# Optimization experiments

Hardware: AMD Instinct MI355X
Metric: run time of the kernel (lower is better)

The kernel has to match this reference:

```python
import jax, jax.numpy as jnp
import numpy as np


def setup_inputs() -> dict:
    key = jax.random.key(0)
    k1, k2, k3 = jax.random.split(key, 3)
    B, C, H, W = 16, 512, 64, 64
    K = 32
    std = 1.0 / (K * C) ** 0.5
    x = jax.random.normal(k1, (B, C, H, W), dtype=jnp.float32)
    codewords = jax.random.uniform(k2, (K, C), dtype=jnp.float32, minval=-std, maxval=std)
    scale = jax.random.uniform(k3, (K,), dtype=jnp.float32, minval=-1.0, maxval=0.0)
    return {"x": x, "codewords": codewords, "scale": scale}


def reference(x, codewords, scale):
    # x: [B, C, H, W] -> tokens [B, N, C] with N = H*W
    B, C, H, W = x.shape
    xf = x.reshape(B, C, H * W).transpose(0, 2, 1)  # [B, N, C]

    # (avoids materializing the [B, N, K, C] tensor the torch code builds)
    x_sq = jnp.sum(xf * xf, axis=-1)                 # [B, N]
    c_sq = jnp.sum(codewords * codewords, axis=-1)   # [K]
    xc = jnp.einsum('bnc,kc->bnk', xf, codewords)    # [B, N, K]
    scaled_l2 = scale * (x_sq[..., None] - 2.0 * xc + c_sq)  # [B, N, K]

    w = jax.nn.softmax(scaled_l2, axis=2)            # [B, N, K]

    # aggregate: sum_n w[b,n,k] * (x[b,n,:] - c[k,:])
    #          = einsum(w, x) - (sum_n w) * c
    enc = jnp.einsum('bnk,bnc->bkc', w, xf) - jnp.sum(w, axis=1)[..., None] * codewords
    return enc  # [B, K, C]
```

## Files before the change

kernel.cpp:

```cpp
#include <hip/hip_runtime.h>


#define B_ 16
#define C_ 512
#define N_ 4096
#define K_ 32
#define CHUNK 64
#define CPB 2
#define BPB (N_ / (CHUNK * CPB))
#define NBLK (B_ * BPB)
#define XCP 72
#define WLS 40

typedef __attribute__((ext_vector_type(8))) short short8;
typedef __attribute__((ext_vector_type(16))) float floatx16;

__device__ inline unsigned short f2bf(float f) {
    union { float f; unsigned u; } v; v.f = f;
    unsigned r = v.u + 0x7FFFu + ((v.u >> 16) & 1u);
    return (unsigned short)(r >> 16);
}

__device__ inline void cbar() {
    __builtin_amdgcn_sched_barrier(0);
    asm volatile("s_waitcnt lgkmcnt(0)" ::: "memory");
    __builtin_amdgcn_s_barrier();
    __builtin_amdgcn_sched_barrier(0);
}

template <int USE_WS>
__global__ __launch_bounds__(256, 2)
void enc_kernel(const float* __restrict__ x,
                const float* __restrict__ cw,
                const float* __restrict__ scale,
                float* __restrict__ outp)
{
    __shared__ unsigned short XC[C_ * XCP];
    __shared__ unsigned short Wl[2][K_ * WLS];
    __shared__ float xsqp[4][CHUNK];
    __shared__ float csq[K_];
    __shared__ float scl[K_];

    const int tid  = threadIdx.x;
    const int wave = tid >> 6;
    const int lane = tid & 63;
    const int l31  = lane & 31;
    const int lh   = lane >> 5;

    const int b    = blockIdx.x >> 5;
    const int pair = blockIdx.x & (BPB - 1);
    const float* xb = x + (long)b * C_ * N_;

    const int r = tid >> 4;
    const int p = tid & 15;

    float4 s0[4], s1[4], s2[4];
#define XISSUE(buf_, ch_, g_)                                                  \
    { _Pragma("unroll")                                                        \
      for (int i = 0; i < 4; ++i)                                              \
          buf_[i] = *(const float4*)(xb + (long)((g_) * 64 + i * 16 + r) * N_  \
                                     + (pair * CPB + (ch_)) * CHUNK + p * 4); }

#define XWRITE(buf_, g_)                                                       \
    { _Pragma("unroll")                                                        \
      for (int i = 0; i < 4; ++i) {                                            \
          const float4 v = buf_[i];                                            \
          xs0 += v.x * v.x; xs1 += v.y * v.y;                                  \
          xs2 += v.z * v.z; xs3 += v.w * v.w;                                  \
          const unsigned lo = (unsigned)f2bf(v.x) | ((unsigned)f2bf(v.y) << 16);\
          const unsigned hi = (unsigned)f2bf(v.z) | ((unsigned)f2bf(v.w) << 16);\
          *(uint2*)&XC[((g_) * 64 + i * 16 + r) * XCP + p * 4] = make_uint2(lo, hi);\
      } }

    const float* cwr = cw + l31 * C_ + lh * 8;
    short8 afA[4], afB[4];
#define AFLOADG(buf_, g_)                                                      \
    { _Pragma("unroll")                                                        \
      for (int s = 0; s < 4; ++s) {                                            \
          const float4 u0 = *(const float4*)(cwr + (g_) * 64 + s * 16);        \
          const float4 u1 = *(const float4*)(cwr + (g_) * 64 + s * 16 + 4);    \
          short8 t_;                                                           \
          t_[0] = (short)f2bf(u0.x); t_[1] = (short)f2bf(u0.y);                \
          t_[2] = (short)f2bf(u0.z); t_[3] = (short)f2bf(u0.w);                \
          t_[4] = (short)f2bf(u1.x); t_[5] = (short)f2bf(u1.y);                \
          t_[6] = (short)f2bf(u1.z); t_[7] = (short)f2bf(u1.w);                \
          buf_[s] = t_; } }

    floatx16 acc[4], wacc;
    #pragma unroll
    for (int t = 0; t < 4; ++t)
        #pragma unroll
        for (int i = 0; i < 16; ++i) acc[t][i] = 0.f;
    #pragma unroll
    for (int i = 0; i < 16; ++i) wacc[i] = 0.f;

    #pragma unroll
    for (int ch = 0; ch < CPB; ++ch) {
        float xs0 = 0.f, xs1 = 0.f, xs2 = 0.f, xs3 = 0.f;

        if (ch == 0) {
            XISSUE(s0, 0, 0)
            XISSUE(s1, 0, 1)
            if (tid < K_) scl[tid] = scale[tid];
            {
                const int k = tid >> 3, q = tid & 7;
                const float4* src = (const float4*)(cw + k * C_ + q * 64);
                float ssum = 0.f;
                #pragma unroll
                for (int i = 0; i < 16; ++i) {
                    const float4 v = src[i];
                    ssum += v.x*v.x + v.y*v.y + v.z*v.z + v.w*v.w;
                }
                ssum += __shfl_xor(ssum, 1);
                ssum += __shfl_xor(ssum, 2);
                ssum += __shfl_xor(ssum, 4);
                if (q == 0) csq[k] = ssum;
            }
            if (wave < 2) AFLOADG(afA, 0)
            XWRITE(s0, 0)
            XISSUE(s2, 0, 2)
        } else {
            if (wave < 2) AFLOADG(afA, 0)
            XWRITE(s0, 0)
        }
        cbar();

        floatx16 S;
        #pragma unroll
        for (int i = 0; i < 16; ++i) S[i] = 0.f;

        #pragma unroll
        for (int g = 0; g < 8; ++g) {
            if (g + 3 < 8) {
                if      ((g % 3) == 0) XISSUE(s0, ch, g + 3)
                else if ((g % 3) == 1) XISSUE(s1, ch, g + 3)
                else                   XISSUE(s2, ch, g + 3)
            }
            if (wave < 2) {
                if (g + 1 < 8) {
                    if (g & 1) AFLOADG(afA, g + 1) else AFLOADG(afB, g + 1)
                }
                #pragma unroll
                for (int s = 0; s < 4; ++s) {
                    short8 bx;
                    #pragma unroll
                    for (int j = 0; j < 8; ++j)
                        bx[j] = (short)XC[(g * 64 + s * 16 + lh * 8 + j) * XCP
                                          + wave * 32 + l31];
                    S = __builtin_amdgcn_mfma_f32_32x32x16_bf16(
                            (g & 1) ? afB[s] : afA[s], bx, S, 0, 0, 0);
                }
            }
            if (g + 1 < 8) {
                if      (((g + 1) % 3) == 0) XWRITE(s0, g + 1)
                else if (((g + 1) % 3) == 1) XWRITE(s1, g + 1)
                else                         XWRITE(s2, g + 1)
            } else if (ch + 1 < CPB) {
                XISSUE(s0, ch + 1, 0)
                XISSUE(s1, ch + 1, 1)
                XISSUE(s2, ch + 1, 2)
            }
            cbar();
        }

        xs0 += __shfl_xor(xs0, 16); xs1 += __shfl_xor(xs1, 16);
        xs2 += __shfl_xor(xs2, 16); xs3 += __shfl_xor(xs3, 16);
        xs0 += __shfl_xor(xs0, 32); xs1 += __shfl_xor(xs1, 32);
        xs2 += __shfl_xor(xs2, 32); xs3 += __shfl_xor(xs3, 32);
        if (lane < 16) {
            xsqp[wave][lane * 4 + 0] = xs0; xsqp[wave][lane * 4 + 1] = xs1;
            xsqp[wave][lane * 4 + 2] = xs2; xsqp[wave][lane * 4 + 3] = xs3;
        }
        cbar();

        if (wave < 2) {
            const int n = wave * 32 + l31;
            const float xq = xsqp[0][n] + xsqp[1][n] + xsqp[2][n] + xsqp[3][n];
            float L[16], mx = -3.4e38f;
            #pragma unroll
            for (int rr = 0; rr < 16; ++rr) {
                const int k = (rr & 3) + 8 * (rr >> 2) + 4 * lh;
                L[rr] = scl[k] * (xq - 2.f * S[rr] + csq[k]);
                mx = fmaxf(mx, L[rr]);
            }
            mx = fmaxf(mx, __shfl_xor(mx, 32));
            float sum = 0.f;
            #pragma unroll
            for (int rr = 0; rr < 16; ++rr) { L[rr] = __expf(L[rr] - mx); sum += L[rr]; }
            sum += __shfl_xor(sum, 32);
            const float inv = 1.f / sum;
            #pragma unroll
            for (int rr = 0; rr < 16; ++rr) {
                const int k = (rr & 3) + 8 * (rr >> 2) + 4 * lh;
                Wl[wave][k * WLS + l31] = f2bf(L[rr] * inv);
            }
        }
        cbar();

        short8 aw[4];
        #pragma unroll
        for (int s = 0; s < 4; ++s)
            aw[s] = *(const short8*)&Wl[s >> 1][l31 * WLS + (s & 1) * 16 + lh * 8];

        {
            short8 ones;
            #pragma unroll
            for (int j = 0; j < 8; ++j) ones[j] = (short)0x3F80;
            #pragma unroll
            for (int s = 0; s < 4; ++s)
                wacc = __builtin_amdgcn_mfma_f32_32x32x16_bf16(aw[s], ones, wacc, 0, 0, 0);
        }

        #pragma unroll
        for (int t = 0; t < 4; ++t) {
            const int c = wave * 128 + t * 32 + l31;
            #pragma unroll
            for (int s = 0; s < 4; ++s) {
                const short8 bx = *(const short8*)&XC[c * XCP + s * 16 + lh * 8];
                acc[t] = __builtin_amdgcn_mfma_f32_32x32x16_bf16(aw[s], bx, acc[t], 0, 0, 0);
            }
        }
        if (ch + 1 < CPB) cbar();
    }

    float* dst = USE_WS ? (outp + (size_t)blockIdx.x * K_ * C_)
                        : (outp + (size_t)b * K_ * C_);
    #pragma unroll
    for (int t = 0; t < 4; ++t) {
        const int c = wave * 128 + t * 32 + l31;
        #pragma unroll
        for (int rr = 0; rr < 16; ++rr) {
            const int k = (rr & 3) + 8 * (rr >> 2) + 4 * lh;
            const float val = acc[t][rr] - wacc[rr] * cw[k * C_ + c];
            if (USE_WS) dst[k * C_ + c] = val;
            else        atomicAdd(dst + k * C_ + c, val);
        }
    }
}

__global__ __launch_bounds__(256)
void reduce_kernel(const float4* __restrict__ part, float4* __restrict__ out)
{
    const int gid = blockIdx.x * 256 + threadIdx.x;
    const int bb  = gid >> 12;
    const int i4  = gid & 4095;
    const float4* pp = part + ((size_t)bb * BPB) * 4096 + i4;
    float4 s = make_float4(0.f, 0.f, 0.f, 0.f);
    #pragma unroll 8
    for (int j = 0; j < BPB; ++j) {
        const float4 v = pp[(size_t)j * 4096];
        s.x += v.x; s.y += v.y; s.z += v.z; s.w += v.w;
    }
    out[gid] = s;
}

extern "C" void kernel_launch(void* const* d_in, const int* in_sizes, int n_in,
                              void* d_out, int out_size, void* d_ws, size_t ws_size,
                              hipStream_t stream) {
    const float* x     = (const float*)d_in[0];
    const float* cw    = (const float*)d_in[1];
    const float* scale = (const float*)d_in[2];
    float* out = (float*)d_out;

    const size_t ws_need = (size_t)NBLK * K_ * C_ * sizeof(float);
    if (ws_size >= ws_need) {
        float* part = (float*)d_ws;
        hipLaunchKernelGGL(enc_kernel<1>, dim3(NBLK), dim3(256), 0, stream,
                           x, cw, scale, part);
        hipLaunchKernelGGL(reduce_kernel, dim3(256), dim3(256), 0, stream,
                           (const float4*)part, (float4*)out);
    } else {
        hipMemsetAsync(out, 0, (size_t)out_size * sizeof(float), stream);
        hipLaunchKernelGGL(enc_kernel<0>, dim3(NBLK), dim3(256), 0, stream,
                           x, cw, scale, out);
    }
}
```

Measured before the change: 227.5 us.

## Shrink LDS to double-buffered slices, split logits across waves, reload x from global

Each block now handles one 64-token chunk instead of two. The full-channel bf16 LDS copy of x is replaced by a two-slice double buffer, so shared memory drops and launch bounds rise to allow 3 blocks per CU. All four waves now compute partial logits, each half covering half of the channels, and the partial sums are combined through shared memory. The second GEMM reloads x from global memory (likely an L2 hit) and converts it to bf16 in registers. This doubles the number of blocks and the partial workspace the reduce kernel must sum, and adds a second global read of x.

```diff
diff --git a/kernel.cpp b/kernel.cpp
--- a/kernel.cpp
+++ b/kernel.cpp
@@ -6,10 +6,9 @@
 #define N_ 4096
 #define K_ 32
 #define CHUNK 64
-#define CPB 2
-#define BPB (N_ / (CHUNK * CPB))
-#define NBLK (B_ * BPB)
-#define XCP 72
+#define NCH (N_ / CHUNK)
+#define NBLK (B_ * NCH)
+#define XCN 68
 #define WLS 40
 
 typedef __attribute__((ext_vector_type(8))) short short8;
@@ -29,15 +28,16 @@
 }
 
 template <int USE_WS>
-__global__ __launch_bounds__(256, 2)
+__global__ __launch_bounds__(256, 3)
 void enc_kernel(const float* __restrict__ x,
                 const float* __restrict__ cw,
                 const float* __restrict__ scale,
                 float* __restrict__ outp)
 {
-    __shared__ unsigned short XC[C_ * XCP];
+    __shared__ unsigned short XC[2][64 * XCN];
+    __shared__ float Sp[4][K_ * 32];
     __shared__ unsigned short Wl[2][K_ * WLS];
-    __shared__ float xsqp[4][CHUNK];
+    __shared__ float xsqL[16][CHUNK];
     __shared__ float csq[K_];
     __shared__ float scl[K_];
 
@@ -46,22 +46,25 @@
     const int lane = tid & 63;
     const int l31  = lane & 31;
     const int lh   = lane >> 5;
-
-    const int b    = blockIdx.x >> 5;
-    const int pair = blockIdx.x & (BPB - 1);
+    const int half = wave >> 1;
+    const int tile = wave & 1;
+
+    const int b     = blockIdx.x >> 6;
+    const int chunk = blockIdx.x & (NCH - 1);
     const float* xb = x + (long)b * C_ * N_;
 
     const int r = tid >> 4;
     const int p = tid & 15;
+    const float* xrow = xb + chunk * CHUNK + p * 4;
 
     float4 s0[4], s1[4], s2[4];
-#define XISSUE(buf_, ch_, g_)                                                  \
+#define XISSUE(buf_, g_)                                                       \
     { _Pragma("unroll")                                                        \
       for (int i = 0; i < 4; ++i)                                              \
-          buf_[i] = *(const float4*)(xb + (long)((g_) * 64 + i * 16 + r) * N_  \
-                                     + (pair * CPB + (ch_)) * CHUNK + p * 4); }
-
-#define XWRITE(buf_, g_)                                                       \
+          buf_[i] = *(const float4*)(xrow + (long)((g_) * 64 + i * 16 + r) * N_); }
+
+    float xs0 = 0.f, xs1 = 0.f, xs2 = 0.f, xs3 = 0.f;
+#define XWRITE(buf_, db_)                                                      \
     { _Pragma("unroll")                                                        \
       for (int i = 0; i < 4; ++i) {                                            \
           const float4 v = buf_[i];                                            \
@@ -69,7 +72,7 @@
           xs2 += v.z * v.z; xs3 += v.w * v.w;                                  \
           const unsigned lo = (unsigned)f2bf(v.x) | ((unsigned)f2bf(v.y) << 16);\
           const unsigned hi = (unsigned)f2bf(v.z) | ((unsigned)f2bf(v.w) << 16);\
-          *(uint2*)&XC[((g_) * 64 + i * 16 + r) * XCP + p * 4] = make_uint2(lo, hi);\
+          *(uint2*)&XC[db_][(i * 16 + r) * XCN + p * 4] = make_uint2(lo, hi);  \
       } }
 
     const float* cwr = cw + l31 * C_ + lh * 8;
@@ -86,141 +89,140 @@
           t_[6] = (short)f2bf(u1.z); t_[7] = (short)f2bf(u1.w);                \
           buf_[s] = t_; } }
 
-    floatx16 acc[4], wacc;
-    #pragma unroll
-    for (int t = 0; t < 4; ++t)
-        #pragma unroll
-        for (int i = 0; i < 16; ++i) acc[t][i] = 0.f;
-    #pragma unroll
-    for (int i = 0; i < 16; ++i) wacc[i] = 0.f;
-
-    #pragma unroll
-    for (int ch = 0; ch < CPB; ++ch) {
-        float xs0 = 0.f, xs1 = 0.f, xs2 = 0.f, xs3 = 0.f;
-
-        if (ch == 0) {
-            XISSUE(s0, 0, 0)
-            XISSUE(s1, 0, 1)
-            if (tid < K_) scl[tid] = scale[tid];
-            {
-                const int k = tid >> 3, q = tid & 7;
-                const float4* src = (const float4*)(cw + k * C_ + q * 64);
-                float ssum = 0.f;
-                #pragma unroll
-                for (int i = 0; i < 16; ++i) {
-                    const float4 v = src[i];
-                    ssum += v.x*v.x + v.y*v.y + v.z*v.z + v.w*v.w;
-                }
-                ssum += __shfl_xor(ssum, 1);
-                ssum += __shfl_xor(ssum, 2);
-                ssum += __shfl_xor(ssum, 4);
-                if (q == 0) csq[k] = ssum;
+    XISSUE(s0, 0)
+    XISSUE(s1, 1)
+    if (tid < K_) scl[tid] = scale[tid];
+    {
+        const int k = tid >> 3, q = tid & 7;
+        const float4* src = (const float4*)(cw + k * C_ + q * 64);
+        float ssum = 0.f;
+        #pragma unroll
+        for (int i = 0; i < 16; ++i) {
+            const float4 v = src[i];
+            ssum += v.x*v.x + v.y*v.y + v.z*v.z + v.w*v.w;
+        }
+        ssum += __shfl_xor(ssum, 1);
+        ssum += __shfl_xor(ssum, 2);
+        ssum += __shfl_xor(ssum, 4);
+        if (q == 0) csq[k] = ssum;
+    }
+    AFLOADG(afA, half * 4)
+    XWRITE(s0, 0)
+    XISSUE(s2, 2)
+    cbar();
+
+    floatx16 S;
+    #pragma unroll
+    for (int i = 0; i < 16; ++i) S[i] = 0.f;
+
+    #pragma unroll
+    for (int g = 0; g < 8; ++g) {
+        if (g + 3 < 8) {
+            if      ((g % 3) == 0) XISSUE(s0, g + 3)
+            else if ((g % 3) == 1) XISSUE(s1, g + 3)
+            else                   XISSUE(s2, g + 3)
+        }
+        if ((g >> 2) == half) {
+            if (((g + 1) >> 2) == half) {
+                if (g & 1) AFLOADG(afA, g + 1) else AFLOADG(afB, g + 1)
             }
-            if (wave < 2) AFLOADG(afA, 0)
-            XWRITE(s0, 0)
-            XISSUE(s2, 0, 2)
-        } else {
-            if (wave < 2) AFLOADG(afA, 0)
-            XWRITE(s0, 0)
-        }
-        cbar();
-
-        floatx16 S;
-        #pragma unroll
-        for (int i = 0; i < 16; ++i) S[i] = 0.f;
-
-        #pragma unroll
-        for (int g = 0; g < 8; ++g) {
-            if (g + 3 < 8) {
-                if      ((g % 3) == 0) XISSUE(s0, ch, g + 3)
-                else if ((g % 3) == 1) XISSUE(s1, ch, g + 3)
-                else                   XISSUE(s2, ch, g + 3)
-            }
-            if (wave < 2) {
-                if (g + 1 < 8) {
-                    if (g & 1) AFLOADG(afA, g + 1) else AFLOADG(afB, g + 1)
-                }
-                #pragma unroll
-                for (int s = 0; s < 4; ++s) {
-                    short8 bx;
-                    #pragma unroll
-                    for (int j = 0; j < 8; ++j)
-                        bx[j] = (short)XC[(g * 64 + s * 16 + lh * 8 + j) * XCP
-                                          + wave * 32 + l31];
-                    S = __builtin_amdgcn_mfma_f32_32x32x16_bf16(
-                            (g & 1) ? afB[s] : afA[s], bx, S, 0, 0, 0);
-                }
-            }
-            if (g + 1 < 8) {
-                if      (((g + 1) % 3) == 0) XWRITE(s0, g + 1)
-                else if (((g + 1) % 3) == 1) XWRITE(s1, g + 1)
-                else                         XWRITE(s2, g + 1)
-            } else if (ch + 1 < CPB) {
-                XISSUE(s0, ch + 1, 0)
-                XISSUE(s1, ch + 1, 1)
-                XISSUE(s2, ch + 1, 2)
-            }
-            cbar();
-        }
-
-        xs0 += __shfl_xor(xs0, 16); xs1 += __shfl_xor(xs1, 16);
-        xs2 += __shfl_xor(xs2, 16); xs3 += __shfl_xor(xs3, 16);
-        xs0 += __shfl_xor(xs0, 32); xs1 += __shfl_xor(xs1, 32);
-        xs2 += __shfl_xor(xs2, 32); xs3 += __shfl_xor(xs3, 32);
-        if (lane < 16) {
-            xsqp[wave][lane * 4 + 0] = xs0; xsqp[wave][lane * 4 + 1] = xs1;
-            xsqp[wave][lane * 4 + 2] = xs2; xsqp[wave][lane * 4 + 3] = xs3;
-        }
-        cbar();
-
-        if (wave < 2) {
-            const int n = wave * 32 + l31;
-            const float xq = xsqp[0][n] + xsqp[1][n] + xsqp[2][n] + xsqp[3][n];
-            float L[16], mx = -3.4e38f;
-            #pragma unroll
-            for (int rr = 0; rr < 16; ++rr) {
-                const int k = (rr & 3) + 8 * (rr >> 2) + 4 * lh;
-                L[rr] = scl[k] * (xq - 2.f * S[rr] + csq[k]);
-                mx = fmaxf(mx, L[rr]);
-            }
-            mx = fmaxf(mx, __shfl_xor(mx, 32));
-            float sum = 0.f;
-            #pragma unroll
-            for (int rr = 0; rr < 16; ++rr) { L[rr] = __expf(L[rr] - mx); sum += L[rr]; }
-            sum += __shfl_xor(sum, 32);
-            const float inv = 1.f / sum;
-            #pragma unroll
-            for (int rr = 0; rr < 16; ++rr) {
-                const int k = (rr & 3) + 8 * (rr >> 2) + 4 * lh;
-                Wl[wave][k * WLS + l31] = f2bf(L[rr] * inv);
-            }
-        }
-        cbar();
-
-        short8 aw[4];
-        #pragma unroll
-        for (int s = 0; s < 4; ++s)
-            aw[s] = *(const short8*)&Wl[s >> 1][l31 * WLS + (s & 1) * 16 + lh * 8];
-
-        {
-            short8 ones;
-            #pragma unroll
-            for (int j = 0; j < 8; ++j) ones[j] = (short)0x3F80;
-            #pragma unroll
-            for (int s = 0; s < 4; ++s)
-                wacc = __builtin_amdgcn_mfma_f32_32x32x16_bf16(aw[s], ones, wacc, 0, 0, 0);
-        }
-
-        #pragma unroll
-        for (int t = 0; t < 4; ++t) {
-            const int c = wave * 128 + t * 32 + l31;
             #pragma unroll
             for (int s = 0; s < 4; ++s) {
-                const short8 bx = *(const short8*)&XC[c * XCP + s * 16 + lh * 8];
-                acc[t] = __builtin_amdgcn_mfma_f32_32x32x16_bf16(aw[s], bx, acc[t], 0, 0, 0);
+                short8 bx;
+                #pragma unroll
+                for (int j = 0; j < 8; ++j)
+                    bx[j] = (short)XC[g & 1][(s * 16 + lh * 8 + j) * XCN
+                                            + tile * 32 + l31];
+                S = __builtin_amdgcn_mfma_f32_32x32x16_bf16(
+                        (g & 1) ? afB[s] : afA[s], bx, S, 0, 0, 0);
             }
         }
-        if (ch + 1 < CPB) cbar();
+        if (g + 1 < 8) {
+            if      (((g + 1) % 3) == 0) XWRITE(s0, (g + 1) & 1)
+            else if (((g + 1) % 3) == 1) XWRITE(s1, (g + 1) & 1)
+            else                         XWRITE(s2, (g + 1) & 1)
+        }
+        cbar();
+    }
+
+    xsqL[r][p * 4 + 0] = xs0; xsqL[r][p * 4 + 1] = xs1;
+    xsqL[r][p * 4 + 2] = xs2; xsqL[r][p * 4 + 3] = xs3;
+    #pragma unroll
+    for (int rr = 0; rr < 16; ++rr)
+        Sp[wave][((rr & 3) + 8 * (rr >> 2) + 4 * lh) * 32 + l31] = S[rr];
+
+    float4 bv[4][2];
+#define G2LOAD(bi_, i_)                                                        \
+    { const int t_ = (i_) >> 2, st_ = (i_) & 3;                                \
+      const int c_ = wave * 128 + t_ * 32 + l31;                               \
+      const int no_ = st_ * 16 + lh * 8;                                       \
+      const float* p_ = xb + (long)c_ * N_ + chunk * CHUNK + no_;              \
+      bv[bi_][0] = *(const float4*)p_;                                         \
+      bv[bi_][1] = *(const float4*)(p_ + 4); }
+    G2LOAD(0, 0)
+    G2LOAD(1, 1)
+    G2LOAD(2, 2)
+    G2LOAD(3, 3)
+    cbar();
+
+    if (wave < 2) {
+        const int n = wave * 32 + l31;
+        float xq = 0.f;
+        #pragma unroll
+        for (int rr = 0; rr < 16; ++rr) xq += xsqL[rr][n];
+        float L[32], mx = -3.4e38f;
+        #pragma unroll
+        for (int k = 0; k < 32; ++k) {
+            const float sv = Sp[wave][k * 32 + l31] + Sp[wave + 2][k * 32 + l31];
+            L[k] = scl[k] * (xq - 2.f * sv + csq[k]);
+            mx = fmaxf(mx, L[k]);
+        }
+        float sum = 0.f;
+        #pragma unroll
+        for (int k = 0; k < 32; ++k) { L[k] = __expf(L[k] - mx); sum += L[k]; }
+        const float inv = 1.f / sum;
+        #pragma unroll
+        for (int k = 0; k < 32; ++k)
+            Wl[wave][k * WLS + l31] = f2bf(L[k] * inv);
+    }
+    cbar();
+
+    short8 aw[4];
+    #pragma unroll
+    for (int s = 0; s < 4; ++s)
+        aw[s] = *(const short8*)&Wl[s >> 1][l31 * WLS + (s & 1) * 16 + lh * 8];
+
+    floatx16 wacc;
+    #pragma unroll
+    for (int i = 0; i < 16; ++i) wacc[i] = 0.f;
+    {
+        short8 ones;
+        #pragma unroll
+        for (int j = 0; j < 8; ++j) ones[j] = (short)0x3F80;
+        #pragma unroll
+        for (int s = 0; s < 4; ++s)
+            wacc = __builtin_amdgcn_mfma_f32_32x32x16_bf16(aw[s], ones, wacc, 0, 0, 0);
+    }
+
+    floatx16 acc[4];
+    #pragma unroll
+    for (int t = 0; t < 4; ++t)
+        #pragma unroll
+        for (int i = 0; i < 16; ++i) acc[t][i] = 0.f;
+
+    #pragma unroll
+    for (int i = 0; i < 16; ++i) {
+        const int bi = i & 3;
+        const int t  = i >> 2, s = i & 3;
+        const float4 v0 = bv[bi][0];
+        const float4 v1 = bv[bi][1];
+        short8 bx;
+        bx[0] = (short)f2bf(v0.x); bx[1] = (short)f2bf(v0.y);
+        bx[2] = (short)f2bf(v0.z); bx[3] = (short)f2bf(v0.w);
+        bx[4] = (short)f2bf(v1.x); bx[5] = (short)f2bf(v1.y);
+        bx[6] = (short)f2bf(v1.z); bx[7] = (short)f2bf(v1.w);
+        acc[t] = __builtin_amdgcn_mfma_f32_32x32x16_bf16(aw[s], bx, acc[t], 0, 0, 0);
+        if (i + 4 < 16) G2LOAD(bi, i + 4)
     }
 
     float* dst = USE_WS ? (outp + (size_t)blockIdx.x * K_ * C_)
@@ -244,10 +246,10 @@
     const int gid = blockIdx.x * 256 + threadIdx.x;
     const int bb  = gid >> 12;
     const int i4  = gid & 4095;
-    const float4* pp = part + ((size_t)bb * BPB) * 4096 + i4;
+    const float4* pp = part + ((size_t)bb * NCH) * 4096 + i4;
     float4 s = make_float4(0.f, 0.f, 0.f, 0.f);
     #pragma unroll 8
-    for (int j = 0; j < BPB; ++j) {
+    for (int j = 0; j < NCH; ++j) {
         const float4 v = pp[(size_t)j * 4096];
         s.x += v.x; s.y += v.y; s.z += v.z; s.w += v.w;
     }
```

Result: slower. 262.8 us (+15.5%).
